# Kernel tuning notes

Measured on AMD Instinct MI355X. Metric: run time of the kernel, lower is better.

## Reference

```python
import jax, jax.numpy as jnp
import numpy as np

B_, L_, D_, R_, N_ = 8, 1024, 512, 32, 16  # batch, seq(in_channels), dim(=dim_inner), dt_rank, d_state


def setup_inputs() -> dict:
    key = jax.random.key(0)
    ks = jax.random.split(key, 8)
    s = lambda k, shape, scale: jax.random.normal(k, shape, dtype=jnp.float32) * scale
    inv = D_ ** -0.5
    return {
        "x": jax.random.uniform(ks[0], (B_, L_, D_), dtype=jnp.float32),
        "W1": s(ks[1], (D_, D_), inv), "b1": jnp.zeros((D_,), jnp.float32),
        "W2": s(ks[2], (D_, D_), inv), "b2": jnp.zeros((D_,), jnp.float32),
        "Wout": s(ks[3], (D_, D_), inv), "bout": jnp.zeros((D_,), jnp.float32),
        "conv_w": s(ks[4], (L_, L_, 3), (3 * L_) ** -0.5),  # Conv1d(L_, L_, k=3) weight (O,I,W)
        "conv_b": jnp.zeros((L_,), jnp.float32),
        "W_dbc": s(ks[5], (R_ + 2 * N_, D_), inv),          # deltaBC projection (no bias)
        "W_dt": s(ks[6], (D_, R_), R_ ** -0.5),             # dt_proj weight
        "b_dt": jnp.zeros((D_,), jnp.float32),
        "A_log": jnp.log(jnp.tile(jnp.arange(1, N_ + 1, dtype=jnp.float32), (D_, 1))),  # (D, N)
        "Dp": jnp.ones((D_,), jnp.float32),
    }


def _silu(v):
    return v * jax.nn.sigmoid(v)


def _selective_scan(u, delta, A, Bm, Cm, Dp):
    # u, delta: (b, l, d); A: (d, n); Bm, Cm: (b, l, n); Dp: (d,)
    dA = jnp.exp(jnp.einsum('bld,dn->bldn', delta, A))          # (b,l,d,n)
    dBu = jnp.einsum('bld,bln,bld->bldn', delta, Bm, u)          # (b,l,d,n)

    def step(h, inp):
        dA_t, dBu_t, C_t = inp                                   # (b,d,n),(b,d,n),(b,n)
        h = dA_t * h + dBu_t
        return h, jnp.einsum('bdn,bn->bd', h, C_t)

    h0 = jnp.zeros((u.shape[0], u.shape[2], A.shape[1]), u.dtype)
    _, ys = jax.lax.scan(step, h0, (dA.transpose(1, 0, 2, 3), dBu.transpose(1, 0, 2, 3), Cm.transpose(1, 0, 2)))
    return ys.transpose(1, 0, 2) + u * Dp                        # (b,l,d)


def reference(x, W1, b1, W2, b2, Wout, bout, conv_w, conv_b, W_dbc, W_dt, b_dt, A_log, Dp):
    skip = x
    x1 = x @ W1.T + b1                                            # proj_one
    x2 = x @ W2.T + b2                                            # proj_two
    # Conv1d over channel axis = L_ (dim 1), spatial axis = D_ (dim 2)
    x1 = jax.lax.conv_general_dilated(x1, conv_w, window_strides=(1,), padding=((1, 1),),
                                      dimension_numbers=('NCW', 'OIW', 'NCW')) + conv_b[None, :, None]
    x1 = _silu(x1)
    # SSM (zeta-style): deltaBC -> split -> dt_proj -> softplus -> selective scan
    dbc = x1 @ W_dbc.T                                            # (b,l,R+2N)
    delta = jax.nn.softplus(dbc[..., :R_] @ W_dt.T + b_dt)        # (b,l,d)
    Bm, Cm = dbc[..., R_:R_ + N_], dbc[..., R_ + N_:]
    A = -jnp.exp(A_log)
    y = _selective_scan(x1, delta, A, Bm, Cm, Dp)
    out = y * _silu(x2) + skip
    return out @ Wout.T + bout
```

## Files before the change

### kernel.cpp

```cpp
#include <hip/hip_runtime.h>
#include <hip/hip_bf16.h>

typedef __hip_bfloat16 bf16;
typedef __bf16 bf16x8 __attribute__((ext_vector_type(8)));
typedef float f32x4 __attribute__((ext_vector_type(4)));

static_assert(sizeof(bf16) == 2, "bf16 must be 2 bytes");

#define NC 32
#define CH 32
#define X1TP_BSTRIDE (514L * 1024)

__device__ __forceinline__ float silu_f(float v) { return v / (1.0f + __expf(-v)); }

__device__ __forceinline__ void gload16(const bf16* g, bf16* l) {
  __builtin_amdgcn_global_load_lds((const __attribute__((address_space(1))) void*)g,
                                   (__attribute__((address_space(3))) void*)l,
                                   16, 0, 0);
}

template <int N> __device__ __forceinline__ void wait_vm() {
  if constexpr (N == 0)      asm volatile("s_waitcnt vmcnt(0)" ::: "memory");
  else if constexpr (N == 4) asm volatile("s_waitcnt vmcnt(4)" ::: "memory");
  else if constexpr (N == 6) asm volatile("s_waitcnt vmcnt(6)" ::: "memory");
  else static_assert(N == 0 || N == 4 || N == 6, "add case");
}

__global__ __launch_bounds__(256) void f2b_kernel(const float* __restrict__ in,
                                                  bf16* __restrict__ out, int n) {
  int i = (blockIdx.x * 256 + threadIdx.x) * 4;
  if (i + 3 < n) {
    float4 v = *reinterpret_cast<const float4*>(in + i);
    ushort4 s;
    s.x = __builtin_bit_cast(unsigned short, __float2bfloat16(v.x));
    s.y = __builtin_bit_cast(unsigned short, __float2bfloat16(v.y));
    s.z = __builtin_bit_cast(unsigned short, __float2bfloat16(v.z));
    s.w = __builtin_bit_cast(unsigned short, __float2bfloat16(v.w));
    *reinterpret_cast<ushort4*>(out + i) = s;
  }
}

__global__ __launch_bounds__(256) void prep_kernel(const float* __restrict__ W1,
                                                   const float* __restrict__ W2,
                                                   const float* __restrict__ Wout,
                                                   const float* __restrict__ Wdbc,
                                                   bf16* __restrict__ w1b, bf16* __restrict__ w2b,
                                                   bf16* __restrict__ woutb, bf16* __restrict__ wdbcb,
                                                   bf16* __restrict__ x1tp) {
  int gid = blockIdx.x * 256 + threadIdx.x;
  int i = gid * 4;
  auto cvt4 = [&](const float* src, bf16* dst) {
    float4 v = *reinterpret_cast<const float4*>(src + i);
    ushort4 s;
    s.x = __builtin_bit_cast(unsigned short, __float2bfloat16(v.x));
    s.y = __builtin_bit_cast(unsigned short, __float2bfloat16(v.y));
    s.z = __builtin_bit_cast(unsigned short, __float2bfloat16(v.z));
    s.w = __builtin_bit_cast(unsigned short, __float2bfloat16(v.w));
    *reinterpret_cast<ushort4*>(dst + i) = s;
  };
  cvt4(W1, w1b);
  cvt4(W2, w2b);
  cvt4(Wout, woutb);
  if (i < 64 * 512) cvt4(Wdbc, wdbcb);
  if (gid < 16384) {
    int b = gid >> 11, rem = gid & 2047;
    int r = rem >> 10, ii = rem & 1023;
    x1tp[(long)b * X1TP_BSTRIDE + (long)r * (513 * 1024) + ii] = __float2bfloat16(0.f);
  }
}

__global__ __launch_bounds__(256) void csplit_kernel(const float* __restrict__ cw,
                                                     bf16* __restrict__ cws) {
  long idx = (long)blockIdx.x * 256 + threadIdx.x;
  int o = (int)(idx >> 10), i = (int)(idx & 1023);
  float a = cw[idx * 3], b = cw[idx * 3 + 1], c = cw[idx * 3 + 2];
  cws[(long)o * 3072 + i]        = __float2bfloat16(a);
  cws[(long)o * 3072 + 1024 + i] = __float2bfloat16(b);
  cws[(long)o * 3072 + 2048 + i] = __float2bfloat16(c);
}

template <int EPI, int BM, int BN, int CONVB, int GX, int GY>
__global__ __launch_bounds__(256) void gemm_nt(const bf16* __restrict__ A,
                                               const bf16* __restrict__ Bw,
                                               const float* __restrict__ bias,
                                               float* __restrict__ outf,
                                               bf16* __restrict__ outb,
                                               int M, int N, int K,
                                               long sAz, long sBz, long sOz) {
  constexpr int BK = 64;
  constexpr int MI = BM / 32, WNF = BN / 32;
  constexpr int APW = BM / 32, BPW = BN / 32;
  constexpr int IPW = APW + BPW;
  __shared__ __align__(16) bf16 As[3][BM * BK];
  __shared__ __align__(16) bf16 Bs[3][BN * BK];

  const int bid = (blockIdx.x & 7) * ((int)gridDim.x >> 3) + (blockIdx.x >> 3);
  const int bx = bid & (GX - 1);
  const int by = (bid / GX) & (GY - 1);
  const int z  = bid / (GX * GY);

  const int tid = threadIdx.x;
  const int w = tid >> 6, l = tid & 63;
  const int wm = w >> 1, wn = w & 1;
  const int m0 = bx * BM, n0 = by * BN;
  const bf16* Ab = A + (long)z * sAz + (long)m0 * K;
  const bf16* Bb = Bw + (long)z * sBz;

  const int lrow = l >> 3;
  const int lcol = (((l & 7) ^ (l >> 3)) << 3);

  auto stage = [&](int buf, int k0) {
#pragma unroll
    for (int j = 0; j < APW; ++j) {
      int iss = w * APW + j;
      int row = iss * 8 + lrow;
      gload16(Ab + (long)row * K + k0 + lcol, &As[buf][iss * 512]);
    }
#pragma unroll
    for (int j = 0; j < BPW; ++j) {
      int iss = w * BPW + j;
      int row = iss * 8 + lrow;
      const bf16* src;
      if (CONVB) src = Bb + (long)(n0 + row + (k0 >> 10)) * 1024 + (k0 & 1023) + lcol;
      else       src = Bb + (long)(n0 + row) * K + k0 + lcol;
      gload16(src, &Bs[buf][iss * 512]);
    }
  };

  f32x4 acc[MI][WNF] = {};
  const int nt = K / BK;
  const int lr = l & 15;
  const int lko = (l >> 4) * 8;
  const int xorm = (lr & 7) << 3;

  stage(0, 0);
  stage(1, BK);
  for (int t = 0; t < nt; ++t) {
    const int cur = t % 3;
    if (t + 1 < nt) wait_vm<IPW>();
    else            wait_vm<0>();
    __builtin_amdgcn_s_barrier();
    __builtin_amdgcn_sched_barrier(0);
#pragma unroll
    for (int kk = 0; kk < 2; ++kk) {
      const int col = (lko + kk * 32) ^ xorm;
      bf16x8 af[MI], bfg[WNF];
#pragma unroll
      for (int mi = 0; mi < MI; ++mi)
        af[mi] = *reinterpret_cast<const bf16x8*>(&As[cur][(wm * (BM / 2) + mi * 16 + lr) * 64 + col]);
#pragma unroll
      for (int ni = 0; ni < WNF; ++ni)
        bfg[ni] = *reinterpret_cast<const bf16x8*>(&Bs[cur][(wn * (BN / 2) + ni * 16 + lr) * 64 + col]);
#pragma unroll
      for (int mi = 0; mi < MI; ++mi)
#pragma unroll
        for (int ni = 0; ni < WNF; ++ni)
          acc[mi][ni] = __builtin_amdgcn_mfma_f32_16x16x32_bf16(af[mi], bfg[ni], acc[mi][ni], 0, 0, 0);
    }
    __builtin_amdgcn_sched_barrier(0);
    __builtin_amdgcn_s_barrier();
    if (t + 2 < nt) stage((t + 2) % 3, (t + 2) * BK);
  }

  const int lq = l >> 4;
#pragma unroll
  for (int mi = 0; mi < MI; ++mi) {
#pragma unroll
    for (int ni = 0; ni < WNF; ++ni) {
#pragma unroll
      for (int j = 0; j < 4; ++j) {
        int m = m0 + wm * (BM / 2) + mi * 16 + lq * 4 + j;
        int n = n0 + wn * (BN / 2) + ni * 16 + lr;
        float v = acc[mi][ni][j];
        if (EPI == 2) {
          v += bias[m];
          (outb + (long)z * sOz)[(long)m * N + n] = __float2bfloat16(silu_f(v));
        } else if (EPI == 3) {
          outf[(long)m * N + n] = v;
        } else if (EPI == 4) {
          v += bias[n];
          outf[(long)m * N + n] = v;
        } else if (EPI == 5) {
          v += bias[m];
          int b = n >> 10, li = n & 1023;
          outb[(long)b * X1TP_BSTRIDE + (long)(m + 1) * 1024 + li] = __float2bfloat16(v);
        } else {
          v += bias[n];
          outb[(long)m * N + n] = __float2bfloat16(silu_f(v));
        }
      }
    }
  }
}

__global__ __launch_bounds__(256) void scan_p1(const bf16* __restrict__ u_bf,
                                               const float* __restrict__ dbc,
                                               const float* __restrict__ W_dt,
                                               const float* __restrict__ b_dt,
                                               const float* __restrict__ A_log,
                                               float* __restrict__ P,
                                               float* __restrict__ Q) {
  const int tid = threadIdx.x;
  const int d = blockIdx.x * 256 + tid;
  const int c = blockIdx.y, b = blockIdx.z;
  __shared__ float sD[CH][64];
  for (int i = tid; i < CH * 64; i += 256) {
    int tt = i >> 6, j = i & 63;
    sD[tt][j] = dbc[((long)b * 1024 + c * CH + tt) * 64 + j];
  }
  __syncthreads();
  float wdt[32];
#pragma unroll
  for (int r = 0; r < 32; r += 4) {
    float4 v = *reinterpret_cast<const float4*>(&W_dt[(long)d * 32 + r]);
    wdt[r] = v.x; wdt[r + 1] = v.y; wdt[r + 2] = v.z; wdt[r + 3] = v.w;
  }
  const float bd = b_dt[d];
  float Adn[16];
#pragma unroll
  for (int n = 0; n < 16; ++n) Adn[n] = -__expf(A_log[d * 16 + n]);
  float p[16], q[16];
#pragma unroll
  for (int n = 0; n < 16; ++n) { p[n] = 1.f; q[n] = 0.f; }
  const long rowb = (long)b * 1024 + c * CH;
  for (int tt = 0; tt < CH; ++tt) {
    float a = bd;
#pragma unroll
    for (int r = 0; r < 32; ++r) a = fmaf(sD[tt][r], wdt[r], a);
    float dv = fmaxf(a, 0.f) + log1pf(__expf(-fabsf(a)));
    float uv = __bfloat162float(u_bf[(rowb + tt) * 512 + d]);
    float s = dv * uv;
#pragma unroll
    for (int n = 0; n < 16; ++n) {
      float dA = __expf(dv * Adn[n]);
      p[n] *= dA;
      q[n] = fmaf(dA, q[n], s * sD[tt][32 + n]);
    }
  }
  float* Pp = P + ((long)b * NC + c) * 8192 + (long)d * 16;
  float* Qp = Q + ((long)b * NC + c) * 8192 + (long)d * 16;
#pragma unroll
  for (int n4 = 0; n4 < 4; ++n4) {
    *reinterpret_cast<float4*>(Pp + n4 * 4) = make_float4(p[n4*4], p[n4*4+1], p[n4*4+2], p[n4*4+3]);
    *reinterpret_cast<float4*>(Qp + n4 * 4) = make_float4(q[n4*4], q[n4*4+1], q[n4*4+2], q[n4*4+3]);
  }
}

__global__ __launch_bounds__(256) void scan_p2(const float* __restrict__ P,
                                               const float* __restrict__ Q,
                                               float* __restrict__ Hin) {
  const int dn = blockIdx.x * 256 + threadIdx.x;
  const int b = blockIdx.y;
  float h = 0.f;
#pragma unroll 4
  for (int c = 0; c < NC; ++c) {
    long idx = ((long)b * NC + c) * 8192 + dn;
    Hin[idx] = h;
    h = fmaf(P[idx], h, Q[idx]);
  }
}

__global__ __launch_bounds__(256) void scan_p3(const bf16* __restrict__ u_bf,
                                               const float* __restrict__ dbc,
                                               const float* __restrict__ W_dt,
                                               const float* __restrict__ b_dt,
                                               const float* __restrict__ A_log,
                                               const float* __restrict__ Dp,
                                               const bf16* __restrict__ x2g,
                                               const bf16* __restrict__ xres,
                                               const float* __restrict__ Hin,
                                               bf16* __restrict__ zb) {
  const int tid = threadIdx.x;
  const int d = blockIdx.x * 256 + tid;
  const int c = blockIdx.y, b = blockIdx.z;
  __shared__ float sD[CH][64];
  for (int i = tid; i < CH * 64; i += 256) {
    int tt = i >> 6, j = i & 63;
    sD[tt][j] = dbc[((long)b * 1024 + c * CH + tt) * 64 + j];
  }
  __syncthreads();
  float wdt[32];
#pragma unroll
  for (int r = 0; r < 32; r += 4) {
    float4 v = *reinterpret_cast<const float4*>(&W_dt[(long)d * 32 + r]);
    wdt[r] = v.x; wdt[r + 1] = v.y; wdt[r + 2] = v.z; wdt[r + 3] = v.w;
  }
  const float bd = b_dt[d];
  float Adn[16];
#pragma unroll
  for (int n = 0; n < 16; ++n) Adn[n] = -__expf(A_log[d * 16 + n]);
  float h[16];
  const float* Hp = Hin + ((long)b * NC + c) * 8192 + (long)d * 16;
#pragma unroll
  for (int n4 = 0; n4 < 4; ++n4) {
    float4 v = *reinterpret_cast<const float4*>(Hp + n4 * 4);
    h[n4*4] = v.x; h[n4*4+1] = v.y; h[n4*4+2] = v.z; h[n4*4+3] = v.w;
  }
  const float Dpv = Dp[d];
  const long rowb = (long)b * 1024 + c * CH;
  for (int tt = 0; tt < CH; ++tt) {
    long off = (rowb + tt) * 512 + d;
    float a = bd;
#pragma unroll
    for (int r = 0; r < 32; ++r) a = fmaf(sD[tt][r], wdt[r], a);
    float dv = fmaxf(a, 0.f) + log1pf(__expf(-fabsf(a)));
    float uv = __bfloat162float(u_bf[off]);
    float s = dv * uv;
    float y = uv * Dpv;
#pragma unroll
    for (int n = 0; n < 16; ++n) {
      float dA = __expf(dv * Adn[n]);
      h[n] = fmaf(dA, h[n], s * sD[tt][32 + n]);
      y = fmaf(h[n], sD[tt][48 + n], y);
    }
    float gate = __bfloat162float(x2g[off]);
    float xv = __bfloat162float(xres[off]);
    zb[off] = __float2bfloat16(fmaf(y, gate, xv));
  }
}

extern "C" void kernel_launch(void* const* d_in, const int* in_sizes, int n_in,
                              void* d_out, int out_size, void* d_ws, size_t ws_size,
                              hipStream_t stream) {
  (void)in_sizes; (void)n_in; (void)out_size; (void)ws_size;
  const float* x    = (const float*)d_in[0];
  const float* W1   = (const float*)d_in[1];
  const float* b1   = (const float*)d_in[2];
  const float* W2   = (const float*)d_in[3];
  const float* b2   = (const float*)d_in[4];
  const float* Wout = (const float*)d_in[5];
  const float* bout = (const float*)d_in[6];
  const float* convw = (const float*)d_in[7];
  const float* convb = (const float*)d_in[8];
  const float* Wdbc = (const float*)d_in[9];
  const float* Wdt  = (const float*)d_in[10];
  const float* bdt  = (const float*)d_in[11];
  const float* Alog = (const float*)d_in[12];
  const float* Dp   = (const float*)d_in[13];
  float* out = (float*)d_out;

  char* ws = (char*)d_ws;
  size_t off = 0;
  auto alloc = [&](size_t bytes) { void* p = ws + off; off += (bytes + 255) & ~(size_t)255; return p; };
  bf16* xb     = (bf16*)alloc(8192L * 512 * 2);
  bf16* w1b    = (bf16*)alloc(512L * 512 * 2);
  bf16* w2b    = (bf16*)alloc(512L * 512 * 2);
  bf16* woutb  = (bf16*)alloc(512L * 512 * 2);
  bf16* wdbcb  = (bf16*)alloc(64L * 512 * 2);
  bf16* cws    = (bf16*)alloc(1024L * 3072 * 2);
  bf16* x1tp   = (bf16*)alloc(8L * X1TP_BSTRIDE * 2);
  bf16* x2g    = (bf16*)alloc(8192L * 512 * 2);
  bf16* x1s    = (bf16*)alloc(8192L * 512 * 2);
  float* dbc   = (float*)alloc(8192L * 64 * 4);
  float* P     = (float*)alloc(8L * NC * 8192 * 4);
  float* Q     = (float*)alloc(8L * NC * 8192 * 4);
  float* Hin   = (float*)alloc(8L * NC * 8192 * 4);
  bf16* zb = xb;

  f2b_kernel<<<8192 * 512 / 1024, 256, 0, stream>>>(x, xb, 8192 * 512);
  prep_kernel<<<256, 256, 0, stream>>>(W1, W2, Wout, Wdbc, w1b, w2b, woutb, wdbcb, x1tp);
  csplit_kernel<<<1024 * 1024 / 256, 256, 0, stream>>>(convw, cws);

  gemm_nt<5, 64, 128, 0, 8, 64><<<512, 256, 0, stream>>>(
      w1b, xb, b1, nullptr, x1tp, 512, 8192, 512, 0, 0, 0);
  gemm_nt<6, 64, 128, 0, 128, 4><<<512, 256, 0, stream>>>(
      xb, w2b, b2, nullptr, x2g, 8192, 512, 512, 0, 0, 0);
  gemm_nt<2, 64, 128, 1, 16, 4><<<512, 256, 0, stream>>>(
      cws, x1tp, convb, nullptr, x1s, 1024, 512, 3072, 0, X1TP_BSTRIDE, 1024L * 512);
  gemm_nt<3, 64, 64, 0, 128, 1><<<128, 256, 0, stream>>>(
      x1s, wdbcb, nullptr, dbc, nullptr, 8192, 64, 512, 0, 0, 0);
  scan_p1<<<dim3(2, NC, 8), 256, 0, stream>>>(x1s, dbc, Wdt, bdt, Alog, P, Q);
  scan_p2<<<dim3(32, 8, 1), 256, 0, stream>>>(P, Q, Hin);
  scan_p3<<<dim3(2, NC, 8), 256, 0, stream>>>(x1s, dbc, Wdt, bdt, Alog, Dp, x2g, xb, Hin, zb);
  gemm_nt<4, 64, 128, 0, 128, 4><<<512, 256, 0, stream>>>(
      zb, woutb, bout, out, nullptr, 8192, 512, 512, 0, 0, 0);
}
```

Before: 177.7 us.

## Merge prep kernels, fuse proj GEMMs, double-buffer with 128x128 tiles

```diff
diff --git a/kernel.cpp b/kernel.cpp
--- a/kernel.cpp
+++ b/kernel.cpp
@@ -22,82 +22,66 @@
 template <int N> __device__ __forceinline__ void wait_vm() {
   if constexpr (N == 0)      asm volatile("s_waitcnt vmcnt(0)" ::: "memory");
   else if constexpr (N == 4) asm volatile("s_waitcnt vmcnt(4)" ::: "memory");
-  else if constexpr (N == 6) asm volatile("s_waitcnt vmcnt(6)" ::: "memory");
-  else static_assert(N == 0 || N == 4 || N == 6, "add case");
-}
-
-__global__ __launch_bounds__(256) void f2b_kernel(const float* __restrict__ in,
-                                                  bf16* __restrict__ out, int n) {
-  int i = (blockIdx.x * 256 + threadIdx.x) * 4;
-  if (i + 3 < n) {
-    float4 v = *reinterpret_cast<const float4*>(in + i);
+  else if constexpr (N == 8) asm volatile("s_waitcnt vmcnt(8)" ::: "memory");
+  else static_assert(N == 0 || N == 4 || N == 8, "add case");
+}
+
+__global__ __launch_bounds__(256) void prep_all(
+    const float* __restrict__ x, const float* __restrict__ W1,
+    const float* __restrict__ W2, const float* __restrict__ Wout,
+    const float* __restrict__ Wdbc, const float* __restrict__ convw,
+    bf16* __restrict__ xb, bf16* __restrict__ w1b, bf16* __restrict__ w2b,
+    bf16* __restrict__ woutb, bf16* __restrict__ wdbcb,
+    bf16* __restrict__ cws, bf16* __restrict__ x1tp) {
+  const int gid = blockIdx.x * 256 + threadIdx.x;
+  auto cvt4 = [](const float* src, bf16* dst, long q) {
+    float4 v = *reinterpret_cast<const float4*>(src + q * 4);
     ushort4 s;
     s.x = __builtin_bit_cast(unsigned short, __float2bfloat16(v.x));
     s.y = __builtin_bit_cast(unsigned short, __float2bfloat16(v.y));
     s.z = __builtin_bit_cast(unsigned short, __float2bfloat16(v.z));
     s.w = __builtin_bit_cast(unsigned short, __float2bfloat16(v.w));
-    *reinterpret_cast<ushort4*>(out + i) = s;
-  }
-}
-
-__global__ __launch_bounds__(256) void prep_kernel(const float* __restrict__ W1,
-                                                   const float* __restrict__ W2,
-                                                   const float* __restrict__ Wout,
-                                                   const float* __restrict__ Wdbc,
-                                                   bf16* __restrict__ w1b, bf16* __restrict__ w2b,
-                                                   bf16* __restrict__ woutb, bf16* __restrict__ wdbcb,
-                                                   bf16* __restrict__ x1tp) {
-  int gid = blockIdx.x * 256 + threadIdx.x;
-  int i = gid * 4;
-  auto cvt4 = [&](const float* src, bf16* dst) {
-    float4 v = *reinterpret_cast<const float4*>(src + i);
-    ushort4 s;
-    s.x = __builtin_bit_cast(unsigned short, __float2bfloat16(v.x));
-    s.y = __builtin_bit_cast(unsigned short, __float2bfloat16(v.y));
-    s.z = __builtin_bit_cast(unsigned short, __float2bfloat16(v.z));
-    s.w = __builtin_bit_cast(unsigned short, __float2bfloat16(v.w));
-    *reinterpret_cast<ushort4*>(dst + i) = s;
+    *reinterpret_cast<ushort4*>(dst + q * 4) = s;
   };
-  cvt4(W1, w1b);
-  cvt4(W2, w2b);
-  cvt4(Wout, woutb);
-  if (i < 64 * 512) cvt4(Wdbc, wdbcb);
-  if (gid < 16384) {
-    int b = gid >> 11, rem = gid & 2047;
+  if (gid < 1048576) {
+    cvt4(x, xb, gid);
+  } else if (gid < 1114112) {
+    cvt4(W1, w1b, gid - 1048576);
+  } else if (gid < 1179648) {
+    cvt4(W2, w2b, gid - 1114112);
+  } else if (gid < 1245184) {
+    cvt4(Wout, woutb, gid - 1179648);
+  } else if (gid < 1253376) {
+    cvt4(Wdbc, wdbcb, gid - 1245184);
+  } else if (gid < 2301952) {
+    long idx = gid - 1253376;
+    int o = (int)(idx >> 10), i = (int)(idx & 1023);
+    float a = convw[idx * 3], b = convw[idx * 3 + 1], c = convw[idx * 3 + 2];
+    cws[(long)o * 3072 + i]        = __float2bfloat16(a);
+    cws[(long)o * 3072 + 1024 + i] = __float2bfloat16(b);
+    cws[(long)o * 3072 + 2048 + i] = __float2bfloat16(c);
+  } else {
+    int e = gid - 2301952;
+    int b = e >> 11, rem = e & 2047;
     int r = rem >> 10, ii = rem & 1023;
     x1tp[(long)b * X1TP_BSTRIDE + (long)r * (513 * 1024) + ii] = __float2bfloat16(0.f);
   }
 }
 
-__global__ __launch_bounds__(256) void csplit_kernel(const float* __restrict__ cw,
-                                                     bf16* __restrict__ cws) {
-  long idx = (long)blockIdx.x * 256 + threadIdx.x;
-  int o = (int)(idx >> 10), i = (int)(idx & 1023);
-  float a = cw[idx * 3], b = cw[idx * 3 + 1], c = cw[idx * 3 + 2];
-  cws[(long)o * 3072 + i]        = __float2bfloat16(a);
-  cws[(long)o * 3072 + 1024 + i] = __float2bfloat16(b);
-  cws[(long)o * 3072 + 2048 + i] = __float2bfloat16(c);
-}
-
-template <int EPI, int BM, int BN, int CONVB, int GX, int GY>
-__global__ __launch_bounds__(256) void gemm_nt(const bf16* __restrict__ A,
-                                               const bf16* __restrict__ Bw,
-                                               const float* __restrict__ bias,
-                                               float* __restrict__ outf,
-                                               bf16* __restrict__ outb,
-                                               int M, int N, int K,
-                                               long sAz, long sBz, long sOz) {
+template <int EPI, int BM, int BN, int CONVB>
+__device__ __forceinline__ void gemm_body(const bf16* __restrict__ A,
+                                          const bf16* __restrict__ Bw,
+                                          const float* __restrict__ bias,
+                                          float* __restrict__ outf,
+                                          bf16* __restrict__ outb,
+                                          int M, int N, int K,
+                                          long sAz, long sBz, long sOz,
+                                          int bx, int by, int z,
+                                          bf16* As, bf16* Bs) {
   constexpr int BK = 64;
   constexpr int MI = BM / 32, WNF = BN / 32;
   constexpr int APW = BM / 32, BPW = BN / 32;
   constexpr int IPW = APW + BPW;
-  __shared__ __align__(16) bf16 As[3][BM * BK];
-  __shared__ __align__(16) bf16 Bs[3][BN * BK];
-
-  const int bid = (blockIdx.x & 7) * ((int)gridDim.x >> 3) + (blockIdx.x >> 3);
-  const int bx = bid & (GX - 1);
-  const int by = (bid / GX) & (GY - 1);
-  const int z  = bid / (GX * GY);
 
   const int tid = threadIdx.x;
   const int w = tid >> 6, l = tid & 63;
@@ -114,7 +98,7 @@
     for (int j = 0; j < APW; ++j) {
       int iss = w * APW + j;
       int row = iss * 8 + lrow;
-      gload16(Ab + (long)row * K + k0 + lcol, &As[buf][iss * 512]);
+      gload16(Ab + (long)row * K + k0 + lcol, &As[buf * BM * 64 + iss * 512]);
     }
 #pragma unroll
     for (int j = 0; j < BPW; ++j) {
@@ -123,7 +107,7 @@
       const bf16* src;
       if (CONVB) src = Bb + (long)(n0 + row + (k0 >> 10)) * 1024 + (k0 & 1023) + lcol;
       else       src = Bb + (long)(n0 + row) * K + k0 + lcol;
-      gload16(src, &Bs[buf][iss * 512]);
+      gload16(src, &Bs[buf * BN * 64 + iss * 512]);
     }
   };
 
@@ -134,10 +118,9 @@
   const int xorm = (lr & 7) << 3;
 
   stage(0, 0);
-  stage(1, BK);
   for (int t = 0; t < nt; ++t) {
-    const int cur = t % 3;
-    if (t + 1 < nt) wait_vm<IPW>();
+    const int cur = t & 1;
+    if (t + 1 < nt) { stage(cur ^ 1, (t + 1) * BK); wait_vm<IPW>(); }
     else            wait_vm<0>();
     __builtin_amdgcn_s_barrier();
     __builtin_amdgcn_sched_barrier(0);
@@ -147,10 +130,12 @@
       bf16x8 af[MI], bfg[WNF];
 #pragma unroll
       for (int mi = 0; mi < MI; ++mi)
-        af[mi] = *reinterpret_cast<const bf16x8*>(&As[cur][(wm * (BM / 2) + mi * 16 + lr) * 64 + col]);
+        af[mi] = *reinterpret_cast<const bf16x8*>(
+            &As[cur * BM * 64 + (wm * (BM / 2) + mi * 16 + lr) * 64 + col]);
 #pragma unroll
       for (int ni = 0; ni < WNF; ++ni)
-        bfg[ni] = *reinterpret_cast<const bf16x8*>(&Bs[cur][(wn * (BN / 2) + ni * 16 + lr) * 64 + col]);
+        bfg[ni] = *reinterpret_cast<const bf16x8*>(
+            &Bs[cur * BN * 64 + (wn * (BN / 2) + ni * 16 + lr) * 64 + col]);
 #pragma unroll
       for (int mi = 0; mi < MI; ++mi)
 #pragma unroll
@@ -159,7 +144,6 @@
     }
     __builtin_amdgcn_sched_barrier(0);
     __builtin_amdgcn_s_barrier();
-    if (t + 2 < nt) stage((t + 2) % 3, (t + 2) * BK);
   }
 
   const int lq = l >> 4;
@@ -193,6 +177,44 @@
   }
 }
 
+template <int EPI, int BM, int BN, int CONVB, int GX, int GY>
+__global__ __launch_bounds__(256) void gemm_nt(const bf16* __restrict__ A,
+                                               const bf16* __restrict__ Bw,
+                                               const float* __restrict__ bias,
+                                               float* __restrict__ outf,
+                                               bf16* __restrict__ outb,
+                                               int M, int N, int K,
+                                               long sAz, long sBz, long sOz) {
+  __shared__ __align__(16) bf16 As[2 * BM * 64];
+  __shared__ __align__(16) bf16 Bs[2 * BN * 64];
+  const int bid = (blockIdx.x & 7) * ((int)gridDim.x >> 3) + (blockIdx.x >> 3);
+  const int by = bid % GY;
+  const int bx = (bid / GY) % GX;
+  const int z  = bid / (GX * GY);
+  gemm_body<EPI, BM, BN, CONVB>(A, Bw, bias, outf, outb, M, N, K, sAz, sBz, sOz,
+                                bx, by, z, As, Bs);
+}
+
+__global__ __launch_bounds__(256) void gemm_dual(
+    const bf16* __restrict__ w1b, const bf16* __restrict__ xb1,
+    const float* __restrict__ b1, bf16* __restrict__ x1tp,
+    const bf16* __restrict__ xb2, const bf16* __restrict__ w2b,
+    const float* __restrict__ b2, bf16* __restrict__ x2g) {
+  __shared__ __align__(16) bf16 As[2 * 128 * 64];
+  __shared__ __align__(16) bf16 Bs[2 * 128 * 64];
+  int bid = (blockIdx.x & 7) * 64 + (blockIdx.x >> 3);
+  if (bid < 256) {
+    int by = bid & 63, bx = bid >> 6;
+    gemm_body<5, 128, 128, 0>(w1b, xb1, b1, nullptr, x1tp, 512, 8192, 512,
+                              0, 0, 0, bx, by, 0, As, Bs);
+  } else {
+    bid -= 256;
+    int by = bid & 3, bx = bid >> 2;
+    gemm_body<6, 128, 128, 0>(xb2, w2b, b2, nullptr, x2g, 8192, 512, 512,
+                              0, 0, 0, bx, by, 0, As, Bs);
+  }
+}
+
 __global__ __launch_bounds__(256) void scan_p1(const bf16* __restrict__ u_bf,
                                                const float* __restrict__ dbc,
                                                const float* __restrict__ W_dt,
@@ -357,21 +379,16 @@
   float* Hin   = (float*)alloc(8L * NC * 8192 * 4);
   bf16* zb = xb;
 
-  f2b_kernel<<<8192 * 512 / 1024, 256, 0, stream>>>(x, xb, 8192 * 512);
-  prep_kernel<<<256, 256, 0, stream>>>(W1, W2, Wout, Wdbc, w1b, w2b, woutb, wdbcb, x1tp);
-  csplit_kernel<<<1024 * 1024 / 256, 256, 0, stream>>>(convw, cws);
-
-  gemm_nt<5, 64, 128, 0, 8, 64><<<512, 256, 0, stream>>>(
-      w1b, xb, b1, nullptr, x1tp, 512, 8192, 512, 0, 0, 0);
-  gemm_nt<6, 64, 128, 0, 128, 4><<<512, 256, 0, stream>>>(
-      xb, w2b, b2, nullptr, x2g, 8192, 512, 512, 0, 0, 0);
-  gemm_nt<2, 64, 128, 1, 16, 4><<<512, 256, 0, stream>>>(
+  prep_all<<<9056, 256, 0, stream>>>(x, W1, W2, Wout, Wdbc, convw,
+                                     xb, w1b, w2b, woutb, wdbcb, cws, x1tp);
+  gemm_dual<<<512, 256, 0, stream>>>(w1b, xb, b1, x1tp, xb, w2b, b2, x2g);
+  gemm_nt<2, 128, 128, 1, 8, 4><<<256, 256, 0, stream>>>(
       cws, x1tp, convb, nullptr, x1s, 1024, 512, 3072, 0, X1TP_BSTRIDE, 1024L * 512);
   gemm_nt<3, 64, 64, 0, 128, 1><<<128, 256, 0, stream>>>(
       x1s, wdbcb, nullptr, dbc, nullptr, 8192, 64, 512, 0, 0, 0);
   scan_p1<<<dim3(2, NC, 8), 256, 0, stream>>>(x1s, dbc, Wdt, bdt, Alog, P, Q);
   scan_p2<<<dim3(32, 8, 1), 256, 0, stream>>>(P, Q, Hin);
   scan_p3<<<dim3(2, NC, 8), 256, 0, stream>>>(x1s, dbc, Wdt, bdt, Alog, Dp, x2g, xb, Hin, zb);
-  gemm_nt<4, 64, 128, 0, 128, 4><<<512, 256, 0, stream>>>(
+  gemm_nt<4, 128, 128, 0, 64, 4><<<256, 256, 0, stream>>>(
       zb, woutb, bout, out, nullptr, 8192, 512, 512, 0, 0, 0);
 }
```

New measurement: 179.6 us. About the same (+1.1%).
